# Performance work log

Hardware: AMD Instinct MI355X
Metric: run time of the kernel (lower is better)

Reference implementation:

```python
import jax, jax.numpy as jnp
import numpy as np

B, S, H, E, V, L = 64, 400, 512, 300, 50000, 1


def setup_inputs() -> dict:
    key = jax.random.key(0)
    ks = jax.random.split(key, 16)
    s = lambda k, shape, fan: jax.random.normal(k, shape, jnp.float32) * (1.0 / np.sqrt(fan))
    return {
        "x": jax.random.randint(ks[0], (B,), 0, V),
        "enc_out": jax.random.normal(ks[1], (B, S, H), jnp.float32),
        "h0": jax.random.normal(ks[2], (L, B, H), jnp.float32),
        "c0": jax.random.normal(ks[3], (L, B, H), jnp.float32),
        "text": jax.random.randint(ks[4], (B, S), 0, V),
        "batch_size": B,
        "emb_table": jax.random.normal(ks[5], (V, E), jnp.float32),
        "V_w": s(ks[6], (1, H), H),
        "V_b": jnp.zeros((1,), jnp.float32),
        "gen_w": s(ks[7], (1, 2 * H + E), 2 * H + E),
        "gen_b": jnp.zeros((1,), jnp.float32),
        "out_w": s(ks[8], (V, 2 * H), 2 * H),
        "out_b": jnp.zeros((V,), jnp.float32),
        "W_ih": s(ks[9], (4 * H, E + H), E + H),
        "W_hh": s(ks[10], (4 * H, H), H),
        "b_ih": jnp.zeros((4 * H,), jnp.float32),
        "b_hh": jnp.zeros((4 * H,), jnp.float32),
    }


def reference(x, enc_out, h0, c0, text, batch_size, emb_table, V_w, V_b,
              gen_w, gen_b, out_w, out_b, W_ih, W_hh, b_ih, b_hh):
    xe = emb_table[x]                                   # [B,E] (dropout off in eval)
    h_prev, c_prev = h0[0], c0[0]                       # [B,H], layers==1
    # Bahdanau attention: V(tanh(enc_out + dec_h)) softmaxed over seq
    score = jnp.tanh(enc_out + h_prev[:, None, :]) @ V_w.T + V_b   # [B,S,1]
    enc_weight = jax.nn.softmax(score, axis=1)                      # [B,S,1]
    ctx = jnp.sum(enc_weight * enc_out, axis=1)                     # [B,H]
    # single-step LSTM cell (torch gate order: i,f,g,o)
    d_in = jnp.concatenate([xe, ctx], axis=-1)                      # [B,E+H]
    gates = d_in @ W_ih.T + h_prev @ W_hh.T + b_ih + b_hh           # [B,4H]
    i, f, g, o = jnp.split(gates, 4, axis=-1)
    c_new = jax.nn.sigmoid(f) * c_prev + jax.nn.sigmoid(i) * jnp.tanh(g)
    h_new = jax.nn.sigmoid(o) * jnp.tanh(c_new)                     # [B,H]
    # pointer-generator combine
    out_cat = jnp.concatenate([h_new, ctx], axis=-1)                # [B,2H]
    gen_in = jnp.concatenate([ctx, h_new, xe], axis=-1)             # [B,2H+E]
    p_gen = jax.nn.sigmoid(gen_in @ gen_w.T + gen_b)[:, 0]          # [B]
    p_ptr = 1.0 - p_gen
    rows = jnp.arange(batch_size)[:, None]                          # [B,1]
    ptr_prob = jnp.zeros((batch_size, out_w.shape[0]), enc_out.dtype)
    ptr_prob = ptr_prob.at[rows, text].set(enc_weight[:, :, 0])     # scatter-set
    gen_prob = out_cat @ out_w.T + out_b                            # [B,V]
    out_prob = p_ptr[:, None] * ptr_prob + p_gen[:, None] * gen_prob
    return out_prob, h_new[None], c_new[None]
```

## Files before the change

kernel.cpp:

```cpp
#include <hip/hip_runtime.h>
#include <hip/hip_bf16.h>

#define BB 64
#define SS 400
#define HH 512
#define EE 300
#define VV 50000
#define KD 812
#define KG 1324
#define KC 1024
#define BV (BB*VV)

typedef __attribute__((ext_vector_type(8))) short bf16x8;
typedef __attribute__((ext_vector_type(4))) float f32x4;
typedef __attribute__((address_space(1))) const void gv_t;
typedef __attribute__((address_space(3))) void lv_t;

#define WS_SCORE 0
#define WS_W     25600
#define WS_CTX   51200
#define WS_HNEW  83968
#define WS_G0    116736
#define WS_G1    247808
#define WS_G2    378880
#define WS_G3    509952
#define WS_PGEN  641024
#define WS_PART  641088
#define WS_ABF   903232
#define WS_AD1   936000
#define WS_AD2   962624

__device__ __forceinline__ float sigm(float x){ return 1.f/(1.f+__expf(-x)); }
__device__ __forceinline__ float ftanh(float x){
  x = fminf(fmaxf(x,-15.f),15.f);
  float e = __expf(2.f*x);
  return (e-1.f)/(e+1.f);
}
__device__ __forceinline__ unsigned short f2bf(float f){
  unsigned int u = __builtin_bit_cast(unsigned int, f);
  u += 0x7fffu + ((u>>16)&1u);
  return (unsigned short)(u>>16);
}

#define LDW(S, off) { w##S##0 = *(const float4*)(wr + (off)*32); \
                      w##S##1 = *(const float4*)(wr + (off)*32 + 4); }
#define LDA(S, off) { a##S##0 = *(const bf16x8*)(a0 + (off)*32); \
                      a##S##1 = *(const bf16x8*)(a1 + (off)*32); \
                      a##S##2 = *(const bf16x8*)(a2 + (off)*32); \
                      a##S##3 = *(const bf16x8*)(a3 + (off)*32); }
#define CONS(S) { union { bf16x8 v; unsigned int u[4]; } bb_; \
  float4 f0_ = w##S##0; float4 f1_ = w##S##1; \
  asm("v_cvt_pk_bf16_f32 %0, %1, %2" : "=v"(bb_.u[0]) : "v"(f0_.x), "v"(f0_.y)); \
  asm("v_cvt_pk_bf16_f32 %0, %1, %2" : "=v"(bb_.u[1]) : "v"(f0_.z), "v"(f0_.w)); \
  asm("v_cvt_pk_bf16_f32 %0, %1, %2" : "=v"(bb_.u[2]) : "v"(f1_.x), "v"(f1_.y)); \
  asm("v_cvt_pk_bf16_f32 %0, %1, %2" : "=v"(bb_.u[3]) : "v"(f1_.z), "v"(f1_.w)); \
  acc0 = __builtin_amdgcn_mfma_f32_16x16x32_bf16(a##S##0, bb_.v, acc0, 0,0,0); \
  acc1 = __builtin_amdgcn_mfma_f32_16x16x32_bf16(a##S##1, bb_.v, acc1, 0,0,0); \
  acc2 = __builtin_amdgcn_mfma_f32_16x16x32_bf16(a##S##2, bb_.v, acc2, 0,0,0); \
  acc3 = __builtin_amdgcn_mfma_f32_16x16x32_bf16(a##S##3, bb_.v, acc3, 0,0,0); }

template<int NSTEP>
__device__ __forceinline__ void mfma_seg2(const float* __restrict__ wr,
    const unsigned short* __restrict__ a0, const unsigned short* __restrict__ a1,
    const unsigned short* __restrict__ a2, const unsigned short* __restrict__ a3,
    f32x4& acc0, f32x4& acc1, f32x4& acc2, f32x4& acc3)
{
  static_assert(NSTEP % 2 == 0 && NSTEP >= 4, "");
  float4 wA0,wA1, wB0,wB1;
  bf16x8 aA0,aA1,aA2,aA3, aB0,aB1,aB2,aB3;
  LDW(A,0) LDA(A,0)
  LDW(B,1) LDA(B,1)
  #pragma unroll
  for (int ks=0; ks<NSTEP; ks+=2){
    CONS(A) if (ks+2 < NSTEP){ LDW(A,ks+2) LDA(A,ks+2) }
    CONS(B) if (ks+3 < NSTEP){ LDW(B,ks+3) LDA(B,ks+3) }
  }
}

__global__ __launch_bounds__(256) void k_prep(const int* __restrict__ x,
    const float* __restrict__ emb, const float* __restrict__ h0,
    unsigned short* __restrict__ ad1, unsigned short* __restrict__ ad2)
{
  int n = blockIdx.x*256 + threadIdx.x;
  if (n < BB*832){
    int b = n/832, k = n - b*832;
    if (k < EE) ad1[n] = f2bf(emb[(size_t)x[b]*EE + k]);
    else if (k >= 812) ad1[n] = 0;
  } else {
    int m = n - BB*832;
    ad2[m] = f2bf(h0[m]);
  }
}

__global__ __launch_bounds__(256) void k_score(const float* __restrict__ enc,
    const float* __restrict__ h0, const float* __restrict__ Vw,
    const float* __restrict__ Vb, float* __restrict__ score)
{
  int wv = threadIdx.x >> 6, lane = threadIdx.x & 63;
  int pair = blockIdx.x*4 + wv;
  int b = pair / SS;
  int i0 = lane*8;
  const float4* ep = (const float4*)(enc + (size_t)pair*HH + i0);
  const float4* hp = (const float4*)(h0 + b*HH + i0);
  const float4* vp = (const float4*)(Vw + i0);
  float4 e0 = ep[0], e1 = ep[1];
  float4 hv0 = hp[0], hv1 = hp[1];
  float4 v0 = vp[0], v1 = vp[1];
  float sum = ftanh(e0.x+hv0.x)*v0.x + ftanh(e0.y+hv0.y)*v0.y
            + ftanh(e0.z+hv0.z)*v0.z + ftanh(e0.w+hv0.w)*v0.w
            + ftanh(e1.x+hv1.x)*v1.x + ftanh(e1.y+hv1.y)*v1.y
            + ftanh(e1.z+hv1.z)*v1.z + ftanh(e1.w+hv1.w)*v1.w;
  #pragma unroll
  for (int off=32; off; off>>=1) sum += __shfl_xor(sum, off);
  if (lane==0) score[pair] = sum + Vb[0];
}

__global__ __launch_bounds__(256) void k_ctx(const float* __restrict__ enc,
    const float* __restrict__ score, float* __restrict__ wout,
    float* __restrict__ part)
{
  __shared__ float red[256];
  __shared__ float wl[SS];
  int b = blockIdx.x >> 3, sp = blockIdx.x & 7;
  int t = threadIdx.x;
  float v1 = score[b*SS + t];
  float v2 = (t < SS-256) ? score[b*SS + t + 256] : -1e30f;
  red[t] = fmaxf(v1, v2);
  __syncthreads();
  for (int o=128; o; o>>=1){ if (t<o) red[t] = fmaxf(red[t], red[t+o]); __syncthreads(); }
  float mx = red[0];
  __syncthreads();
  float e1 = __expf(v1 - mx);
  float e2 = (t < SS-256) ? __expf(v2 - mx) : 0.f;
  red[t] = e1 + e2;
  __syncthreads();
  for (int o=128; o; o>>=1){ if (t<o) red[t] += red[t+o]; __syncthreads(); }
  float inv = 1.f/red[0];
  float w1 = e1*inv;
  wl[t] = w1;
  if (sp==0) wout[b*SS + t] = w1;
  if (t < SS-256){
    float w2 = e2*inv;
    wl[t+256] = w2;
    if (sp==0) wout[b*SS + t + 256] = w2;
  }
  __syncthreads();
  float a0 = 0.f, a1 = 0.f;
  const float* ebase = enc + ((size_t)b*SS + sp*50)*HH + 2*t;
  #pragma unroll 5
  for (int s=0; s<50; ++s){
    float wg = wl[sp*50 + s];
    float2 e = *(const float2*)(ebase + s*HH);
    a0 += wg * e.x;
    a1 += wg * e.y;
  }
  *(float2*)(part + (size_t)(b*8+sp)*HH + 2*t) = make_float2(a0, a1);
}

__global__ __launch_bounds__(256) void k_ctx_reduce(const float* __restrict__ part,
    float* __restrict__ ctx, unsigned short* __restrict__ ad1)
{
  int b = blockIdx.x, t = threadIdx.x;
  float a0=0.f, a1=0.f;
  #pragma unroll
  for (int sp=0; sp<8; ++sp){
    float2 e = *(const float2*)(part + (size_t)(b*8+sp)*HH + 2*t);
    a0 += e.x; a1 += e.y;
  }
  *(float2*)(ctx + b*HH + 2*t) = make_float2(a0, a1);
  ad1[b*832 + EE + 2*t]     = f2bf(a0);
  ad1[b*832 + EE + 2*t + 1] = f2bf(a1);
}

__global__ __launch_bounds__(128, 4) void k_gates(const float* __restrict__ Wih,
    const float* __restrict__ Whh, const unsigned short* __restrict__ ad1,
    const unsigned short* __restrict__ ad2,
    float* __restrict__ g0, float* __restrict__ g1,
    float* __restrict__ g2, float* __restrict__ g3)
{
  int wt = blockIdx.x*2 + (threadIdx.x >> 6);
  int lane = threadIdx.x & 63;
  int col = lane & 15, kg = lane >> 4;
  int jt = wt >> 2, part = wt & 3;
  int j = jt*16 + col;
  f32x4 acc0={0.f,0.f,0.f,0.f}, acc1=acc0, acc2=acc0, acc3=acc0;
  float* g;
  if (part < 2){
    int k0 = part ? 384 : 0;
    const float* wr = Wih + (size_t)j*KD + k0 + kg*8;
    const unsigned short* a = ad1 + col*832 + k0 + kg*8;
    if (part) mfma_seg2<14>(wr, a, a+16*832, a+32*832, a+48*832, acc0,acc1,acc2,acc3);
    else      mfma_seg2<12>(wr, a, a+16*832, a+32*832, a+48*832, acc0,acc1,acc2,acc3);
    g = part ? g1 : g0;
  } else {
    int k0 = (part==3) ? 256 : 0;
    const float* wr = Whh + (size_t)j*HH + k0 + kg*8;
    const unsigned short* a = ad2 + col*512 + k0 + kg*8;
    mfma_seg2<8>(wr, a, a+16*512, a+32*512, a+48*512, acc0,acc1,acc2,acc3);
    g = (part==3) ? g3 : g2;
  }
  #pragma unroll
  for (int i=0;i<4;i++){
    g[(size_t)j*BB + 0*16 + kg*4 + i] = acc0[i];
    g[(size_t)j*BB + 1*16 + kg*4 + i] = acc1[i];
    g[(size_t)j*BB + 2*16 + kg*4 + i] = acc2[i];
    g[(size_t)j*BB + 3*16 + kg*4 + i] = acc3[i];
  }
}

__global__ __launch_bounds__(256) void k_lstm(const float* __restrict__ c0,
    const float* __restrict__ bih, const float* __restrict__ bhh,
    const float* __restrict__ g0, const float* __restrict__ g1,
    const float* __restrict__ g2, const float* __restrict__ g3,
    const float* __restrict__ ctx, float* __restrict__ hnew,
    unsigned short* __restrict__ abf, float* __restrict__ out)
{
  int n = blockIdx.x*256 + threadIdx.x;
  int b = n & 63, h = n >> 6;
  #define GSUM(off) (g0[(off)*BB+b] + g1[(off)*BB+b] + g2[(off)*BB+b] + g3[(off)*BB+b] + bih[off] + bhh[off])
  float gi = GSUM(h);
  float gf = GSUM(HH+h);
  float gg = GSUM(2*HH+h);
  float go = GSUM(3*HH+h);
  #undef GSUM
  float cn = sigm(gf)*c0[b*HH+h] + sigm(gi)*ftanh(gg);
  float hn = sigm(go)*ftanh(cn);
  out[BV + b*HH + h]          = hn;
  out[BV + BB*HH + b*HH + h]  = cn;
  hnew[b*HH + h] = hn;
  abf[b*KC + h]      = f2bf(hn);
  abf[b*KC + HH + h] = f2bf(ctx[b*HH + h]);
}

__global__ __launch_bounds__(256) void k_pgen(const float* __restrict__ genw,
    const float* __restrict__ genb, const float* __restrict__ ctx,
    const float* __restrict__ hnew, const int* __restrict__ x,
    const float* __restrict__ emb, float* __restrict__ pgen)
{
  __shared__ float red[256];
  int b = blockIdx.x, t = threadIdx.x;
  float p = 0.f;
  for (int k=t; k<KG; k+=256){
    float g = genw[k];
    float v = (k < HH) ? ctx[b*HH + k]
            : (k < 2*HH) ? hnew[b*HH + k - HH]
            : emb[(size_t)x[b]*EE + (k - 2*HH)];
    p += g*v;
  }
  red[t] = p; __syncthreads();
  for (int o=128; o; o>>=1){ if (t<o) red[t] += red[t+o]; __syncthreads(); }
  if (t==0) pgen[b] = sigm(red[0] + genb[0]);
}

#define PADB 4112
__global__ __launch_bounds__(512, 4) void k_gemm(const float* __restrict__ out_w,
    const float* __restrict__ out_b, const unsigned short* __restrict__ abf,
    const float* __restrict__ pgen, float* __restrict__ out)
{
  __shared__ __align__(16) char wlds[16*PADB];
  __shared__ float comb[4][16][17];
  int t = threadIdx.x;
  int w = t >> 6, lane = t & 63;
  int col = lane & 15, kg = lane >> 4;
  int vt = blockIdx.x;
  int mt = w >> 1, kh = w & 1;
  const char* wbase = (const char*)(out_w + (size_t)vt*16*KC);

  #pragma unroll
  for (int i=0;i<8;i++){
    int c = w*8 + i;
    int r = c >> 2, q = c & 3;
    const char* gp = wbase + r*4096 + q*1024 + lane*16;
    __builtin_amdgcn_global_load_lds((gv_t*)gp, (lv_t*)(wlds + r*PADB + q*1024), 16, 0, 0);
  }

  const unsigned short* ap = abf + (size_t)(mt*16 + col)*KC + kh*512 + kg*8;
  bf16x8 pa[16];
  #pragma unroll
  for (int ks=0; ks<16; ++ks) pa[ks] = *(const bf16x8*)(ap + ks*32);

  __syncthreads();

  const char* rb = wlds + col*PADB + kh*2048 + kg*32;
  f32x4 acc = {0.f,0.f,0.f,0.f};
  #pragma unroll
  for (int ks=0; ks<16; ++ks){
    float4 f0 = *(const float4*)(rb + ks*128);
    float4 f1 = *(const float4*)(rb + ks*128 + 16);
    union { bf16x8 v; unsigned int u[4]; } bb;
    asm("v_cvt_pk_bf16_f32 %0, %1, %2" : "=v"(bb.u[0]) : "v"(f0.x), "v"(f0.y));
    asm("v_cvt_pk_bf16_f32 %0, %1, %2" : "=v"(bb.u[1]) : "v"(f0.z), "v"(f0.w));
    asm("v_cvt_pk_bf16_f32 %0, %1, %2" : "=v"(bb.u[2]) : "v"(f1.x), "v"(f1.y));
    asm("v_cvt_pk_bf16_f32 %0, %1, %2" : "=v"(bb.u[3]) : "v"(f1.z), "v"(f1.w));
    acc = __builtin_amdgcn_mfma_f32_16x16x32_bf16(pa[ks], bb.v, acc, 0,0,0);
  }

  if (kh == 1){
    #pragma unroll
    for (int i=0;i<4;i++) comb[mt][kg*4 + i][col] = acc[i];
  }
  __syncthreads();
  if (kh == 0){
    int v = vt*16 + col;
    float ob = out_b[v];
    #pragma unroll
    for (int i=0;i<4;i++){
      int b = mt*16 + kg*4 + i;
      out[(size_t)b*VV + v] = pgen[b]*(acc[i] + comb[mt][kg*4 + i][col] + ob);
    }
  }
}

__global__ __launch_bounds__(256) void k_scatter(const int* __restrict__ text,
    const float* __restrict__ w, const float* __restrict__ pgen,
    float* __restrict__ out)
{
  __shared__ int ts[SS];
  int b = blockIdx.x, t = threadIdx.x;
  ts[t] = text[b*SS + t];
  if (t + 256 < SS) ts[t+256] = text[b*SS + t + 256];
  __syncthreads();
  float pp = 1.f - pgen[b];
  #pragma unroll
  for (int rep=0; rep<2; ++rep){
    int s = t + rep*256;
    if (s < SS){
      int v = ts[s];
      bool dup = false;
      #pragma unroll 4
      for (int s2=s+1; s2<SS; ++s2) dup = dup || (ts[s2]==v);
      if (!dup) out[(size_t)b*VV + v] += pp * w[b*SS + s];
    }
  }
}

extern "C" void kernel_launch(void* const* d_in, const int* in_sizes, int n_in,
                              void* d_out, int out_size, void* d_ws, size_t ws_size,
                              hipStream_t stream)
{
  const int*   x    = (const int*)  d_in[0];
  const float* enc  = (const float*)d_in[1];
  const float* h0   = (const float*)d_in[2];
  const float* c0   = (const float*)d_in[3];
  const int*   text = (const int*)  d_in[4];
  const float* emb  = (const float*)d_in[6];
  const float* Vw   = (const float*)d_in[7];
  const float* Vb   = (const float*)d_in[8];
  const float* genw = (const float*)d_in[9];
  const float* genb = (const float*)d_in[10];
  const float* outw = (const float*)d_in[11];
  const float* outb = (const float*)d_in[12];
  const float* Wih  = (const float*)d_in[13];
  const float* Whh  = (const float*)d_in[14];
  const float* bih  = (const float*)d_in[15];
  const float* bhh  = (const float*)d_in[16];
  float* out = (float*)d_out;

  float* ws     = (float*)d_ws;
  float* score  = ws + WS_SCORE;
  float* wbuf   = ws + WS_W;
  float* ctx    = ws + WS_CTX;
  float* hnew   = ws + WS_HNEW;
  float* g0     = ws + WS_G0;
  float* g1     = ws + WS_G1;
  float* g2     = ws + WS_G2;
  float* g3     = ws + WS_G3;
  float* pgen   = ws + WS_PGEN;
  float* part   = ws + WS_PART;
  unsigned short* abf = (unsigned short*)(ws + WS_ABF);
  unsigned short* ad1 = (unsigned short*)(ws + WS_AD1);
  unsigned short* ad2 = (unsigned short*)(ws + WS_AD2);

  k_prep<<<336, 256, 0, stream>>>(x, emb, h0, ad1, ad2);
  k_score<<<6400, 256, 0, stream>>>(enc, h0, Vw, Vb, score);
  k_ctx<<<512, 256, 0, stream>>>(enc, score, wbuf, part);
  k_ctx_reduce<<<64, 256, 0, stream>>>(part, ctx, ad1);
  k_gates<<<256, 128, 0, stream>>>(Wih, Whh, ad1, ad2, g0, g1, g2, g3);
  k_lstm<<<128, 256, 0, stream>>>(c0, bih, bhh, g0, g1, g2, g3, ctx, hnew, abf, out);
  k_pgen<<<64, 256, 0, stream>>>(genw, genb, ctx, hnew, x, emb, pgen);
  k_gemm<<<3125, 512, 0, stream>>>(outw, outb, abf, pgen, out);
  k_scatter<<<64, 256, 0, stream>>>(text, wbuf, pgen, out);
}
```

Before: 144.2 us.

## Make output GEMM persistent with double-buffered LDS weight prefetch

The output-projection GEMM now launches 256 persistent blocks instead of one block per 16-column tile. Each block walks a contiguous range of roughly 12 tiles and prefetches the next tile's weights into a second LDS buffer while computing the current one. The activation fragments are loaded once per block instead of once per tile. This aims to hide global-to-LDS latency and cut per-block launch and setup cost, but it doubles LDS use and lowers occupancy to two blocks per CU. Using only 256 blocks may also leave the weight stream short of the in-flight memory traffic it needs.

```diff
diff --git a/kernel.cpp b/kernel.cpp
--- a/kernel.cpp
+++ b/kernel.cpp
@@ -253,62 +253,76 @@
 }
 
 #define PADB 4112
-__global__ __launch_bounds__(512, 4) void k_gemm(const float* __restrict__ out_w,
+__global__ __launch_bounds__(512, 2) void k_gemm(const float* __restrict__ out_w,
     const float* __restrict__ out_b, const unsigned short* __restrict__ abf,
     const float* __restrict__ pgen, float* __restrict__ out)
 {
-  __shared__ __align__(16) char wlds[16*PADB];
+  __shared__ __align__(16) char wlds[2][16*PADB];
   __shared__ float comb[4][16][17];
   int t = threadIdx.x;
   int w = t >> 6, lane = t & 63;
   int col = lane & 15, kg = lane >> 4;
-  int vt = blockIdx.x;
   int mt = w >> 1, kh = w & 1;
-  const char* wbase = (const char*)(out_w + (size_t)vt*16*KC);
-
-  #pragma unroll
-  for (int i=0;i<8;i++){
-    int c = w*8 + i;
-    int r = c >> 2, q = c & 3;
-    const char* gp = wbase + r*4096 + q*1024 + lane*16;
-    __builtin_amdgcn_global_load_lds((gv_t*)gp, (lv_t*)(wlds + r*PADB + q*1024), 16, 0, 0);
-  }
+  int bid = blockIdx.x;
+  int ts = (bid * 3125) >> 8;
+  int te = ((bid + 1) * 3125) >> 8;
 
   const unsigned short* ap = abf + (size_t)(mt*16 + col)*KC + kh*512 + kg*8;
   bf16x8 pa[16];
   #pragma unroll
   for (int ks=0; ks<16; ++ks) pa[ks] = *(const bf16x8*)(ap + ks*32);
 
-  __syncthreads();
-
-  const char* rb = wlds + col*PADB + kh*2048 + kg*32;
-  f32x4 acc = {0.f,0.f,0.f,0.f};
-  #pragma unroll
-  for (int ks=0; ks<16; ++ks){
-    float4 f0 = *(const float4*)(rb + ks*128);
-    float4 f1 = *(const float4*)(rb + ks*128 + 16);
-    union { bf16x8 v; unsigned int u[4]; } bb;
-    asm("v_cvt_pk_bf16_f32 %0, %1, %2" : "=v"(bb.u[0]) : "v"(f0.x), "v"(f0.y));
-    asm("v_cvt_pk_bf16_f32 %0, %1, %2" : "=v"(bb.u[1]) : "v"(f0.z), "v"(f0.w));
-    asm("v_cvt_pk_bf16_f32 %0, %1, %2" : "=v"(bb.u[2]) : "v"(f1.x), "v"(f1.y));
-    asm("v_cvt_pk_bf16_f32 %0, %1, %2" : "=v"(bb.u[3]) : "v"(f1.z), "v"(f1.w));
-    acc = __builtin_amdgcn_mfma_f32_16x16x32_bf16(pa[ks], bb.v, acc, 0,0,0);
-  }
-
-  if (kh == 1){
+  #define DMASTAGE(buf_, tile_) { \
+    const char* wb_ = (const char*)(out_w + (size_t)(tile_)*16*KC); \
+    _Pragma("unroll") \
+    for (int i_=0;i_<8;i_++){ \
+      int c_ = w*8 + i_; \
+      int r_ = c_ >> 2, q_ = c_ & 3; \
+      __builtin_amdgcn_global_load_lds( \
+        (gv_t*)(wb_ + r_*4096 + q_*1024 + lane*16), \
+        (lv_t*)(&wlds[buf_][0] + r_*PADB + q_*1024), 16, 0, 0); \
+    } }
+
+  DMASTAGE(0, ts)
+  int cur = 0;
+  for (int tile = ts; tile < te; ++tile){
+    __syncthreads();
+    if (tile + 1 < te) DMASTAGE(cur^1, tile+1)
+
+    const char* rb = &wlds[cur][0] + col*PADB + kh*2048 + kg*32;
+    f32x4 acc = {0.f,0.f,0.f,0.f};
     #pragma unroll
-    for (int i=0;i<4;i++) comb[mt][kg*4 + i][col] = acc[i];
-  }
-  __syncthreads();
-  if (kh == 0){
-    int v = vt*16 + col;
-    float ob = out_b[v];
-    #pragma unroll
-    for (int i=0;i<4;i++){
-      int b = mt*16 + kg*4 + i;
-      out[(size_t)b*VV + v] = pgen[b]*(acc[i] + comb[mt][kg*4 + i][col] + ob);
+    for (int ks=0; ks<16; ++ks){
+      float4 f0 = *(const float4*)(rb + ks*128);
+      float4 f1 = *(const float4*)(rb + ks*128 + 16);
+      union { bf16x8 v; unsigned int u[4]; } bb;
+      asm("v_cvt_pk_bf16_f32 %0, %1, %2" : "=v"(bb.u[0]) : "v"(f0.x), "v"(f0.y));
+      asm("v_cvt_pk_bf16_f32 %0, %1, %2" : "=v"(bb.u[1]) : "v"(f0.z), "v"(f0.w));
+      asm("v_cvt_pk_bf16_f32 %0, %1, %2" : "=v"(bb.u[2]) : "v"(f1.x), "v"(f1.y));
+      asm("v_cvt_pk_bf16_f32 %0, %1, %2" : "=v"(bb.u[3]) : "v"(f1.z), "v"(f1.w));
+      acc = __builtin_amdgcn_mfma_f32_16x16x32_bf16(pa[ks], bb.v, acc, 0,0,0);
     }
-  }
+
+    if (kh == 1){
+      #pragma unroll
+      for (int i=0;i<4;i++) comb[mt][kg*4 + i][col] = acc[i];
+    }
+    asm volatile("s_waitcnt lgkmcnt(0)");
+    __builtin_amdgcn_sched_barrier(0);
+    __builtin_amdgcn_s_barrier();
+    __builtin_amdgcn_sched_barrier(0);
+    if (kh == 0){
+      int v = tile*16 + col;
+      float ob = out_b[v];
+      #pragma unroll
+      for (int i=0;i<4;i++){
+        int b = mt*16 + kg*4 + i;
+        out[(size_t)b*VV + v] = pgen[b]*(acc[i] + comb[mt][kg*4 + i][col] + ob);
+      }
+    }
+    cur ^= 1;
+  }
+  #undef DMASTAGE
 }
 
 __global__ __launch_bounds__(256) void k_scatter(const int* __restrict__ text,
@@ -378,6 +392,6 @@
   k_gates<<<256, 128, 0, stream>>>(Wih, Whh, ad1, ad2, g0, g1, g2, g3);
   k_lstm<<<128, 256, 0, stream>>>(c0, bih, bhh, g0, g1, g2, g3, ctx, hnew, abf, out);
   k_pgen<<<64, 256, 0, stream>>>(genw, genb, ctx, hnew, x, emb, pgen);
-  k_gemm<<<3125, 512, 0, stream>>>(outw, outb, abf, pgen, out);
+  k_gemm<<<256, 512, 0, stream>>>(outw, outb, abf, pgen, out);
   k_scatter<<<64, 256, 0, stream>>>(text, wbuf, pgen, out);
 }
```

After: 129.3 us. 10.3% less time.
